# Optimization experiments

Measured on AMD Instinct MI355X. Metric: run time of the kernel, lower is better.

## Reference

```python
import jax, jax.numpy as jnp
import numpy as np

B, N = 1, 320  # embed_dim == seq_len == N is forced by the module's bmm shapes


def setup_inputs() -> dict:
    key = jax.random.key(0)
    k1, k2, k3, k4 = jax.random.split(key, 4)
    s = jax.random.normal(k1, (B, N, N), dtype=jnp.float32)
    futrue = jax.random.normal(k2, (B, N, N, N), dtype=jnp.float32)
    # nn.Linear(embed_dim, embed_dim) params
    lim = 1.0 / np.sqrt(N)
    W = jax.random.uniform(k3, (N, N), minval=-lim, maxval=lim, dtype=jnp.float32)
    b = jax.random.uniform(k4, (N,), minval=-lim, maxval=lim, dtype=jnp.float32)
    return {"s": s, "futrue": futrue, "W": W, "b": b}


def reference(s, futrue, W, b):
    # futrue = self.fc(futrue): Linear on last dim  [B,T,T,E]
    futP = jnp.einsum('bitj,ej->bite', futrue, W) + b
    # fc = s.transpose(1,2) @ futrue : [B,1,E,T] @ [B,T,T,E] -> [B,T,E,E]
    scores = jnp.einsum('bte,bitj->biej', s, futP)
    fc = jax.nn.softmax(scores, axis=-1)          # softmax over last dim
    # vectorized loop: t_i = fc[:, i].sum(1).unsqueeze(-2).bmm(s)
    w = fc.sum(axis=2)                            # [B, T, T] (sum over e)
    out = jnp.einsum('bij,bjk->bik', w, s)        # concat of all t_i -> [B, T, E]
    return out
```

## Files before the change

### kernel.cpp

```cpp
#include <hip/hip_runtime.h>
#include <hip/hip_bf16.h>
#include <math.h>

#define N 320
#define NN (N * N)
#define SST 324

typedef float f32x16 __attribute__((ext_vector_type(16)));
typedef short s16x8  __attribute__((ext_vector_type(8)));

#define MFMA32(a, b, c) __builtin_amdgcn_mfma_f32_32x32x16_bf16((a), (b), (c), 0, 0, 0)

union U4V { uint4 q; s16x8 v; };
union UAV { unsigned u[4]; s16x8 v; };

__device__ inline void split2(float x0, float x1, unsigned& hi, unsigned& lo) {
    unsigned u0 = __float_as_uint(x0), u1 = __float_as_uint(x1);
    hi = (u0 >> 16) | (u1 & 0xFFFF0000u);
    float d0 = x0 - __uint_as_float(u0 & 0xFFFF0000u);
    float d1 = x1 - __uint_as_float(u1 & 0xFFFF0000u);
    lo = (__float_as_uint(d0) >> 16) | (__float_as_uint(d1) & 0xFFFF0000u);
}

__global__ __launch_bounds__(256) void prep_kernel(
    const float* __restrict__ s, const float* __restrict__ W,
    float* __restrict__ wbuf, float* __restrict__ out, float* __restrict__ colsum,
    uint4* __restrict__ spH, uint4* __restrict__ spL,
    uint4* __restrict__ wpH, uint4* __restrict__ wpL)
{
    const int bid = blockIdx.x;
    const int tid = threadIdx.x;
    if (bid < 100) {
        ((float4*)wbuf)[bid * 256 + tid] = make_float4(0.f, 0.f, 0.f, 0.f);
    } else if (bid < 200) {
        ((float4*)out)[(bid - 100) * 256 + tid] = make_float4(0.f, 0.f, 0.f, 0.f);
    } else if (bid < 202) {
        int e = (bid - 200) * 256 + tid;
        if (e < N) {
            const float* sp = s + e;
            float a[8];
#pragma unroll
            for (int u = 0; u < 8; ++u) a[u] = 0.f;
            for (int t = 0; t < N; t += 8) {
#pragma unroll
                for (int u = 0; u < 8; ++u) a[u] += sp[(size_t)(t + u) * N];
            }
            colsum[e] = ((a[0] + a[1]) + (a[2] + a[3])) + ((a[4] + a[5]) + (a[6] + a[7]));
        }
    } else if (bid < 252) {
        int sub = (bid - 202) * 4 + (tid >> 6);
        int l = tid & 63;
        int et = sub / 20, ts = sub % 20;
        int e = et * 32 + (l & 31);
        int t0 = ts * 16 + (l >> 5) * 8;
        unsigned hi[4], lo[4];
#pragma unroll
        for (int d = 0; d < 4; ++d)
            split2(s[(size_t)(t0 + 2 * d) * N + e], s[(size_t)(t0 + 2 * d + 1) * N + e],
                   hi[d], lo[d]);
        spH[sub * 64 + l] = make_uint4(hi[0], hi[1], hi[2], hi[3]);
        spL[sub * 64 + l] = make_uint4(lo[0], lo[1], lo[2], lo[3]);
    } else {
        int sub = (bid - 252) * 4 + (tid >> 6);
        int l = tid & 63;
        int jt = sub / 20, ks = sub % 20;
        int j = jt * 32 + (l & 31);
        int k0 = ks * 16 + (l >> 5) * 8;
        const float* wr = W + (size_t)j * N + k0;
        unsigned hi[4], lo[4];
#pragma unroll
        for (int d = 0; d < 4; ++d) split2(wr[2 * d], wr[2 * d + 1], hi[d], lo[d]);
        wpH[sub * 64 + l] = make_uint4(hi[0], hi[1], hi[2], hi[3]);
        wpL[sub * 64 + l] = make_uint4(lo[0], lo[1], lo[2], lo[3]);
    }
}

__global__ __launch_bounds__(640, 5) void fused5_kernel(
    const float* __restrict__ fut,
    const uint4* __restrict__ spH, const uint4* __restrict__ spL,
    const uint4* __restrict__ wpH, const uint4* __restrict__ wpL,
    const float* __restrict__ bvec, const float* __restrict__ colsum,
    float* __restrict__ w)
{
    const int bid = blockIdx.x;
    const int x  = bid & 7;
    const int g  = bid >> 3;
    const int iw = g / 5, eq = g % 5;
    const int i  = iw * 8 + x;
    const int tid = threadIdx.x;
    const int wid = tid >> 6;
    const int lane = tid & 63;
    const int l31 = lane & 31;
    const int hf  = lane >> 5;

    __shared__ union {
        unsigned short G[2][40 * 32 * 8];
        float S[32 * SST];
    } sm;
    __shared__ float csh[64];
    __shared__ float Mfin[32];
    __shared__ float Ifin[32];

    if (tid < 64) csh[tid] = colsum[eq * 64 + tid];

    f32x16 acc0, acc1;
#pragma unroll
    for (int r = 0; r < 16; ++r) { acc0[r] = 0.f; acc1[r] = 0.f; }

    const float* fbase = fut + (size_t)i * NN + (size_t)(hf * 8) * N + wid * 32 + l31;
    const uint4* aH0 = spH + (size_t)((eq * 2 + 0) * 20) * 64 + lane;
    const uint4* aL0 = spL + (size_t)((eq * 2 + 0) * 20) * 64 + lane;
    const uint4* aH1 = spH + (size_t)((eq * 2 + 1) * 20) * 64 + lane;
    const uint4* aL1 = spL + (size_t)((eq * 2 + 1) * 20) * 64 + lane;

#pragma unroll 2
    for (int ts = 0; ts < 20; ++ts) {
        const float* fp = fbase + (size_t)(ts * 16) * N;
        float f[8];
#pragma unroll
        for (int m = 0; m < 8; ++m) f[m] = fp[(size_t)m * N];
        UAV bh, bl;
#pragma unroll
        for (int d = 0; d < 4; ++d) split2(f[2 * d], f[2 * d + 1], bh.u[d], bl.u[d]);
        U4V a0h, a0l, a1h, a1l;
        a0h.q = aH0[ts * 64]; a0l.q = aL0[ts * 64];
        a1h.q = aH1[ts * 64]; a1l.q = aL1[ts * 64];
        acc0 = MFMA32(a0h.v, bh.v, acc0);
        acc1 = MFMA32(a1h.v, bh.v, acc1);
        acc0 = MFMA32(a0l.v, bh.v, acc0);
        acc1 = MFMA32(a1l.v, bh.v, acc1);
        acc0 = MFMA32(a0h.v, bl.v, acc0);
        acc1 = MFMA32(a1h.v, bl.v, acc1);
    }

    const uint4* bHp = wpH + (size_t)(wid * 20) * 64 + lane;
    const uint4* bLp = wpL + (size_t)(wid * 20) * 64 + lane;
    const int jcol = wid * 32 + l31;
    const float bj = bvec[jcol];
    const int hw = tid >> 5;
    const int li = tid & 31;
    float wcol = 0.f;

    auto doSlab = [&](const f32x16& acc, const int slab) {
        {
            const int c  = wid * 4 + (l31 >> 3);
            const int jj = l31 & 7;
            const int sw = c & 7;
            unsigned short* GH = sm.G[0];
            unsigned short* GL = sm.G[1];
#pragma unroll
            for (int r = 0; r < 16; ++r) {
                int e = (r & 3) + ((r >> 2) << 3) + (hf << 2);
                float xv = acc[r];
                unsigned u = __float_as_uint(xv);
                float d = xv - __uint_as_float(u & 0xFFFF0000u);
                int off = (c * 32 + (e ^ sw)) * 8 + jj;
                GH[off] = (unsigned short)(u >> 16);
                GL[off] = (unsigned short)(__float_as_uint(d) >> 16);
            }
        }
        __syncthreads();

        f32x16 p;
#pragma unroll
        for (int r = 0; r < 16; ++r) p[r] = 0.f;
        const unsigned short* GH = sm.G[0];
        const unsigned short* GL = sm.G[1];
#pragma unroll 4
        for (int ks = 0; ks < 20; ++ks) {
            int c = ks * 2 + hf;
            int off = (c * 32 + (l31 ^ (c & 7))) * 8;
            s16x8 gh = *(const s16x8*)&GH[off];
            s16x8 gl = *(const s16x8*)&GL[off];
            U4V wh, wl;
            wh.q = bHp[ks * 64];
            wl.q = bLp[ks * 64];
            p = MFMA32(gh, wh.v, p);
            p = MFMA32(gl, wh.v, p);
            p = MFMA32(gh, wl.v, p);
        }

        float v[16];
#pragma unroll
        for (int r = 0; r < 16; ++r) {
            int e = (r & 3) + ((r >> 2) << 3) + (hf << 2);
            v[r] = p[r] + csh[slab * 32 + e] * bj;
        }
        __syncthreads();

#pragma unroll
        for (int r = 0; r < 16; ++r) {
            int e = (r & 3) + ((r >> 2) << 3) + (hf << 2);
            sm.S[e * SST + jcol] = v[r];
        }
        __syncthreads();

        if (hw < 16) {
#pragma unroll
            for (int rr = 0; rr < 2; ++rr) {
                int row = 2 * hw + rr;
                float xr[10];
                float m = -3.4e38f;
#pragma unroll
                for (int q = 0; q < 10; ++q) {
                    xr[q] = sm.S[row * SST + li + 32 * q];
                    m = fmaxf(m, xr[q]);
                }
#pragma unroll
                for (int off = 16; off; off >>= 1) m = fmaxf(m, __shfl_xor(m, off, 64));
                float ssum = 0.f;
#pragma unroll
                for (int q = 0; q < 10; ++q) ssum += __expf(xr[q] - m);
#pragma unroll
                for (int off = 16; off; off >>= 1) ssum += __shfl_xor(ssum, off, 64);
                if (li == 0) { Mfin[row] = m; Ifin[row] = 1.0f / ssum; }
            }
        }
        __syncthreads();

#pragma unroll
        for (int r = 0; r < 16; ++r) {
            int e = (r & 3) + ((r >> 2) << 3) + (hf << 2);
            wcol += __expf(v[r] - Mfin[e]) * Ifin[e];
        }
    };

    doSlab(acc0, 0);
    doSlab(acc1, 1);

    wcol += __shfl_xor(wcol, 32, 64);
    if (hf == 0) atomicAdd(&w[(size_t)i * N + jcol], wcol);
}

__global__ __launch_bounds__(320) void out_gemm_kernel(
    const float* __restrict__ w, const float* __restrict__ s,
    float* __restrict__ out)
{
    const int i = blockIdx.x;
    const int jc = blockIdx.y;
    const int k = threadIdx.x;
    const float* wr = w + (size_t)i * N + jc * 80;
    const float* sp = s + (size_t)(jc * 80) * N + k;
    float a0 = 0.f, a1 = 0.f, a2 = 0.f, a3 = 0.f;
    for (int j = 0; j < 80; j += 4) {
        a0 += wr[j + 0] * sp[(size_t)(j + 0) * N];
        a1 += wr[j + 1] * sp[(size_t)(j + 1) * N];
        a2 += wr[j + 2] * sp[(size_t)(j + 2) * N];
        a3 += wr[j + 3] * sp[(size_t)(j + 3) * N];
    }
    atomicAdd(&out[(size_t)i * N + k], (a0 + a1) + (a2 + a3));
}

extern "C" void kernel_launch(void* const* d_in, const int* in_sizes, int n_in,
                              void* d_out, int out_size, void* d_ws, size_t ws_size,
                              hipStream_t stream)
{
    const float* s    = (const float*)d_in[0];
    const float* fut  = (const float*)d_in[1];
    const float* W    = (const float*)d_in[2];
    const float* bvec = (const float*)d_in[3];
    float* out = (float*)d_out;

    char* base = (char*)d_ws;
    float* wbuf   = (float*)base;
    float* colsum = (float*)(base + 409600);
    uint4* spH = (uint4*)(base + 410880);
    uint4* spL = (uint4*)(base + 615680);
    uint4* wpH = (uint4*)(base + 820480);
    uint4* wpL = (uint4*)(base + 1025280);

    prep_kernel<<<dim3(302), dim3(256), 0, stream>>>(
        s, W, wbuf, out, colsum, spH, spL, wpH, wpL);

    fused5_kernel<<<dim3(1600), dim3(640), 0, stream>>>(
        fut, spH, spL, wpH, wpL, bvec, colsum, wbuf);

    out_gemm_kernel<<<dim3(N, 4), dim3(320), 0, stream>>>(wbuf, s, out);
}
```

Baseline: 414.7 us.

## Pre-pack futrue into bf16 hi/lo MFMA fragments in a separate kernel

Adds a packf kernel that reads futrue through shared memory and writes it once as bf16 hi/lo split fragments already in MFMA operand layout. The fused kernel then loads packed fragments instead of doing strided fp32 loads and splitting per block. Each block now handles one 32-row e-tile instead of two, so twice as many blocks run, and the split-precision products use separate accumulators. The cost is an extra 131 MB round-trip (packed hi+lo written then re-read), and each packed fragment is re-read by 10 blocks.

```diff
diff --git a/kernel.cpp b/kernel.cpp
--- a/kernel.cpp
+++ b/kernel.cpp
@@ -12,7 +12,6 @@
 #define MFMA32(a, b, c) __builtin_amdgcn_mfma_f32_32x32x16_bf16((a), (b), (c), 0, 0, 0)
 
 union U4V { uint4 q; s16x8 v; };
-union UAV { unsigned u[4]; s16x8 v; };
 
 __device__ inline void split2(float x0, float x1, unsigned& hi, unsigned& lo) {
     unsigned u0 = __float_as_uint(x0), u1 = __float_as_uint(x1);
@@ -75,18 +74,54 @@
     }
 }
 
-__global__ __launch_bounds__(640, 5) void fused5_kernel(
+__global__ __launch_bounds__(320) void packf_kernel(
     const float* __restrict__ fut,
+    uint4* __restrict__ fpH, uint4* __restrict__ fpL)
+{
+    const int bid = blockIdx.x;
+    const int i = bid / 5, tq = bid % 5;
+    const int t = threadIdx.x;
+    const int l = t & 63, l31 = l & 31, hf = l >> 5;
+    const int jt0 = t >> 6;
+
+    __shared__ float ld[16 * 320];
+
+    for (int tt = 0; tt < 4; ++tt) {
+        const int ts = tq * 4 + tt;
+        const float4* src = (const float4*)(fut + (size_t)i * NN + (size_t)ts * 16 * N);
+        if (tt) __syncthreads();
+#pragma unroll
+        for (int rep = 0; rep < 4; ++rep)
+            ((float4*)ld)[rep * 320 + t] = src[rep * 320 + t];
+        __syncthreads();
+#pragma unroll
+        for (int rr = 0; rr < 2; ++rr) {
+            const int jt = jt0 + rr * 5;
+            const int j = jt * 32 + l31;
+            unsigned hi[4], lo[4];
+#pragma unroll
+            for (int d = 0; d < 4; ++d) {
+                float x0 = ld[(hf * 8 + 2 * d) * 320 + j];
+                float x1 = ld[(hf * 8 + 2 * d + 1) * 320 + j];
+                split2(x0, x1, hi[d], lo[d]);
+            }
+            size_t sub = (size_t)(i * 10 + jt) * 20 + ts;
+            fpH[sub * 64 + l] = make_uint4(hi[0], hi[1], hi[2], hi[3]);
+            fpL[sub * 64 + l] = make_uint4(lo[0], lo[1], lo[2], lo[3]);
+        }
+    }
+}
+
+__global__ __launch_bounds__(640, 5) void fused_kernel(
+    const uint4* __restrict__ fpH, const uint4* __restrict__ fpL,
     const uint4* __restrict__ spH, const uint4* __restrict__ spL,
     const uint4* __restrict__ wpH, const uint4* __restrict__ wpL,
     const float* __restrict__ bvec, const float* __restrict__ colsum,
     float* __restrict__ w)
 {
     const int bid = blockIdx.x;
-    const int x  = bid & 7;
-    const int g  = bid >> 3;
-    const int iw = g / 5, eq = g % 5;
-    const int i  = iw * 8 + x;
+    const int i   = (bid / 80) * 8 + (bid & 7);
+    const int et  = (bid >> 3) % 10;
     const int tid = threadIdx.x;
     const int wid = tid >> 6;
     const int lane = tid & 63;
@@ -97,137 +132,124 @@
         unsigned short G[2][40 * 32 * 8];
         float S[32 * SST];
     } sm;
-    __shared__ float csh[64];
+    __shared__ float csh[32];
     __shared__ float Mfin[32];
     __shared__ float Ifin[32];
 
-    if (tid < 64) csh[tid] = colsum[eq * 64 + tid];
-
-    f32x16 acc0, acc1;
-#pragma unroll
-    for (int r = 0; r < 16; ++r) { acc0[r] = 0.f; acc1[r] = 0.f; }
-
-    const float* fbase = fut + (size_t)i * NN + (size_t)(hf * 8) * N + wid * 32 + l31;
-    const uint4* aH0 = spH + (size_t)((eq * 2 + 0) * 20) * 64 + lane;
-    const uint4* aL0 = spL + (size_t)((eq * 2 + 0) * 20) * 64 + lane;
-    const uint4* aH1 = spH + (size_t)((eq * 2 + 1) * 20) * 64 + lane;
-    const uint4* aL1 = spL + (size_t)((eq * 2 + 1) * 20) * 64 + lane;
+    if (tid < 32) csh[tid] = colsum[et * 32 + tid];
+
+    f32x16 acc1, acc2;
+#pragma unroll
+    for (int r = 0; r < 16; ++r) { acc1[r] = 0.f; acc2[r] = 0.f; }
+
+    const uint4* fH  = fpH + (size_t)((i * 10 + wid) * 20) * 64 + lane;
+    const uint4* fL  = fpL + (size_t)((i * 10 + wid) * 20) * 64 + lane;
+    const uint4* aHp = spH + (size_t)(et * 20) * 64 + lane;
+    const uint4* aLp = spL + (size_t)(et * 20) * 64 + lane;
 
 #pragma unroll 2
     for (int ts = 0; ts < 20; ++ts) {
-        const float* fp = fbase + (size_t)(ts * 16) * N;
-        float f[8];
-#pragma unroll
-        for (int m = 0; m < 8; ++m) f[m] = fp[(size_t)m * N];
-        UAV bh, bl;
-#pragma unroll
-        for (int d = 0; d < 4; ++d) split2(f[2 * d], f[2 * d + 1], bh.u[d], bl.u[d]);
-        U4V a0h, a0l, a1h, a1l;
-        a0h.q = aH0[ts * 64]; a0l.q = aL0[ts * 64];
-        a1h.q = aH1[ts * 64]; a1l.q = aL1[ts * 64];
-        acc0 = MFMA32(a0h.v, bh.v, acc0);
-        acc1 = MFMA32(a1h.v, bh.v, acc1);
-        acc0 = MFMA32(a0l.v, bh.v, acc0);
-        acc1 = MFMA32(a1l.v, bh.v, acc1);
-        acc0 = MFMA32(a0h.v, bl.v, acc0);
-        acc1 = MFMA32(a1h.v, bl.v, acc1);
-    }
+        U4V ah, al, bh, bl;
+        ah.q = aHp[ts * 64];
+        al.q = aLp[ts * 64];
+        bh.q = fH[ts * 64];
+        bl.q = fL[ts * 64];
+        acc1 = MFMA32(ah.v, bh.v, acc1);
+        acc2 = MFMA32(al.v, bh.v, acc2);
+        acc2 = MFMA32(ah.v, bl.v, acc2);
+    }
+
+    {
+        const int c  = wid * 4 + (l31 >> 3);
+        const int jj = l31 & 7;
+        const int sw = c & 7;
+        unsigned short* GH = sm.G[0];
+        unsigned short* GL = sm.G[1];
+#pragma unroll
+        for (int r = 0; r < 16; ++r) {
+            int e = (r & 3) + ((r >> 2) << 3) + (hf << 2);
+            float x = acc1[r] + acc2[r];
+            unsigned u = __float_as_uint(x);
+            float d = x - __uint_as_float(u & 0xFFFF0000u);
+            int off = (c * 32 + (e ^ sw)) * 8 + jj;
+            GH[off] = (unsigned short)(u >> 16);
+            GL[off] = (unsigned short)(__float_as_uint(d) >> 16);
+        }
+    }
+    __syncthreads();
+
+    f32x16 p1, p2;
+#pragma unroll
+    for (int r = 0; r < 16; ++r) { p1[r] = 0.f; p2[r] = 0.f; }
 
     const uint4* bHp = wpH + (size_t)(wid * 20) * 64 + lane;
     const uint4* bLp = wpL + (size_t)(wid * 20) * 64 + lane;
+    const unsigned short* GH = sm.G[0];
+    const unsigned short* GL = sm.G[1];
+
+#pragma unroll 4
+    for (int ks = 0; ks < 20; ++ks) {
+        int c = ks * 2 + hf;
+        int off = (c * 32 + (l31 ^ (c & 7))) * 8;
+        s16x8 gh = *(const s16x8*)&GH[off];
+        s16x8 gl = *(const s16x8*)&GL[off];
+        U4V wh, wl;
+        wh.q = bHp[ks * 64];
+        wl.q = bLp[ks * 64];
+        p1 = MFMA32(gh, wh.v, p1);
+        p2 = MFMA32(gl, wh.v, p2);
+        p2 = MFMA32(gh, wl.v, p2);
+    }
+
     const int jcol = wid * 32 + l31;
-    const float bj = bvec[jcol];
+    float bj = bvec[jcol];
+    float v[16];
+#pragma unroll
+    for (int r = 0; r < 16; ++r) {
+        int e = (r & 3) + ((r >> 2) << 3) + (hf << 2);
+        v[r] = (p1[r] + p2[r]) + csh[e] * bj;
+    }
+
+    __syncthreads();
+
+#pragma unroll
+    for (int r = 0; r < 16; ++r) {
+        int e = (r & 3) + ((r >> 2) << 3) + (hf << 2);
+        sm.S[e * SST + jcol] = v[r];
+    }
+    __syncthreads();
+
     const int hw = tid >> 5;
     const int li = tid & 31;
+    if (hw < 16) {
+#pragma unroll
+        for (int rr = 0; rr < 2; ++rr) {
+            int row = 2 * hw + rr;
+            float x[10];
+            float m = -3.4e38f;
+#pragma unroll
+            for (int q = 0; q < 10; ++q) {
+                x[q] = sm.S[row * SST + li + 32 * q];
+                m = fmaxf(m, x[q]);
+            }
+#pragma unroll
+            for (int off = 16; off; off >>= 1) m = fmaxf(m, __shfl_xor(m, off, 64));
+            float ssum = 0.f;
+#pragma unroll
+            for (int q = 0; q < 10; ++q) ssum += __expf(x[q] - m);
+#pragma unroll
+            for (int off = 16; off; off >>= 1) ssum += __shfl_xor(ssum, off, 64);
+            if (li == 0) { Mfin[row] = m; Ifin[row] = 1.0f / ssum; }
+        }
+    }
+    __syncthreads();
+
     float wcol = 0.f;
-
-    auto doSlab = [&](const f32x16& acc, const int slab) {
-        {
-            const int c  = wid * 4 + (l31 >> 3);
-            const int jj = l31 & 7;
-            const int sw = c & 7;
-            unsigned short* GH = sm.G[0];
-            unsigned short* GL = sm.G[1];
-#pragma unroll
-            for (int r = 0; r < 16; ++r) {
-                int e = (r & 3) + ((r >> 2) << 3) + (hf << 2);
-                float xv = acc[r];
-                unsigned u = __float_as_uint(xv);
-                float d = xv - __uint_as_float(u & 0xFFFF0000u);
-                int off = (c * 32 + (e ^ sw)) * 8 + jj;
-                GH[off] = (unsigned short)(u >> 16);
-                GL[off] = (unsigned short)(__float_as_uint(d) >> 16);
-            }
-        }
-        __syncthreads();
-
-        f32x16 p;
-#pragma unroll
-        for (int r = 0; r < 16; ++r) p[r] = 0.f;
-        const unsigned short* GH = sm.G[0];
-        const unsigned short* GL = sm.G[1];
-#pragma unroll 4
-        for (int ks = 0; ks < 20; ++ks) {
-            int c = ks * 2 + hf;
-            int off = (c * 32 + (l31 ^ (c & 7))) * 8;
-            s16x8 gh = *(const s16x8*)&GH[off];
-            s16x8 gl = *(const s16x8*)&GL[off];
-            U4V wh, wl;
-            wh.q = bHp[ks * 64];
-            wl.q = bLp[ks * 64];
-            p = MFMA32(gh, wh.v, p);
-            p = MFMA32(gl, wh.v, p);
-            p = MFMA32(gh, wl.v, p);
-        }
-
-        float v[16];
-#pragma unroll
-        for (int r = 0; r < 16; ++r) {
-            int e = (r & 3) + ((r >> 2) << 3) + (hf << 2);
-            v[r] = p[r] + csh[slab * 32 + e] * bj;
-        }
-        __syncthreads();
-
-#pragma unroll
-        for (int r = 0; r < 16; ++r) {
-            int e = (r & 3) + ((r >> 2) << 3) + (hf << 2);
-            sm.S[e * SST + jcol] = v[r];
-        }
-        __syncthreads();
-
-        if (hw < 16) {
-#pragma unroll
-            for (int rr = 0; rr < 2; ++rr) {
-                int row = 2 * hw + rr;
-                float xr[10];
-                float m = -3.4e38f;
-#pragma unroll
-                for (int q = 0; q < 10; ++q) {
-                    xr[q] = sm.S[row * SST + li + 32 * q];
-                    m = fmaxf(m, xr[q]);
-                }
-#pragma unroll
-                for (int off = 16; off; off >>= 1) m = fmaxf(m, __shfl_xor(m, off, 64));
-                float ssum = 0.f;
-#pragma unroll
-                for (int q = 0; q < 10; ++q) ssum += __expf(xr[q] - m);
-#pragma unroll
-                for (int off = 16; off; off >>= 1) ssum += __shfl_xor(ssum, off, 64);
-                if (li == 0) { Mfin[row] = m; Ifin[row] = 1.0f / ssum; }
-            }
-        }
-        __syncthreads();
-
-#pragma unroll
-        for (int r = 0; r < 16; ++r) {
-            int e = (r & 3) + ((r >> 2) << 3) + (hf << 2);
-            wcol += __expf(v[r] - Mfin[e]) * Ifin[e];
-        }
-    };
-
-    doSlab(acc0, 0);
-    doSlab(acc1, 1);
-
+#pragma unroll
+    for (int r = 0; r < 16; ++r) {
+        int e = (r & 3) + ((r >> 2) << 3) + (hf << 2);
+        wcol += __expf(v[r] - Mfin[e]) * Ifin[e];
+    }
     wcol += __shfl_xor(wcol, 32, 64);
     if (hf == 0) atomicAdd(&w[(size_t)i * N + jcol], wcol);
 }
@@ -268,12 +290,16 @@
     uint4* spL = (uint4*)(base + 615680);
     uint4* wpH = (uint4*)(base + 820480);
     uint4* wpL = (uint4*)(base + 1025280);
+    uint4* fpH = (uint4*)(base + 1230080);
+    uint4* fpL = (uint4*)(base + 1230080 + 65536000);
 
     prep_kernel<<<dim3(302), dim3(256), 0, stream>>>(
         s, W, wbuf, out, colsum, spH, spL, wpH, wpL);
 
-    fused5_kernel<<<dim3(1600), dim3(640), 0, stream>>>(
-        fut, spH, spL, wpH, wpL, bvec, colsum, wbuf);
+    packf_kernel<<<dim3(1600), dim3(320), 0, stream>>>(fut, fpH, fpL);
+
+    fused_kernel<<<dim3(3200), dim3(640), 0, stream>>>(
+        fpH, fpL, spH, spL, wpH, wpL, bvec, colsum, wbuf);
 
     out_gemm_kernel<<<dim3(N, 4), dim3(320), 0, stream>>>(wbuf, s, out);
 }
```

Result: slower. 429.2 us (+3.5%).

## Process both 32-row slabs together to halve barriers and softmax passes

Applied to the files above, without the earlier changes.

Merges the two sequential per-slab passes (split to bf16, projection GEMM, softmax stats) into one pass over all 64 rows, using 80KB of dynamic shared memory that holds both slabs' hi/lo planes and then a 64x320 score tile. This cuts the number of __syncthreads and lets the projection MFMAs of both slabs interleave with separate accumulators for more ILP. In exchange, shared memory per block roughly doubles and launch bounds drop from 5 to 4 blocks per CU, which lowers occupancy. The padded row stride is also removed, which may add LDS bank conflicts.

```diff
diff --git a/kernel.cpp b/kernel.cpp
--- a/kernel.cpp
+++ b/kernel.cpp
@@ -4,7 +4,6 @@
 
 #define N 320
 #define NN (N * N)
-#define SST 324
 
 typedef float f32x16 __attribute__((ext_vector_type(16)));
 typedef short s16x8  __attribute__((ext_vector_type(8)));
@@ -75,13 +74,17 @@
     }
 }
 
-__global__ __launch_bounds__(640, 5) void fused5_kernel(
+__global__ __launch_bounds__(640, 4) void fused64_kernel(
     const float* __restrict__ fut,
     const uint4* __restrict__ spH, const uint4* __restrict__ spL,
     const uint4* __restrict__ wpH, const uint4* __restrict__ wpL,
     const float* __restrict__ bvec, const float* __restrict__ colsum,
     float* __restrict__ w)
 {
+    extern __shared__ char smraw[];
+    unsigned short* Gsh = (unsigned short*)smraw;
+    float* Ssh = (float*)smraw;
+
     const int bid = blockIdx.x;
     const int x  = bid & 7;
     const int g  = bid >> 3;
@@ -93,16 +96,6 @@
     const int l31 = lane & 31;
     const int hf  = lane >> 5;
 
-    __shared__ union {
-        unsigned short G[2][40 * 32 * 8];
-        float S[32 * SST];
-    } sm;
-    __shared__ float csh[64];
-    __shared__ float Mfin[32];
-    __shared__ float Ifin[32];
-
-    if (tid < 64) csh[tid] = colsum[eq * 64 + tid];
-
     f32x16 acc0, acc1;
 #pragma unroll
     for (int r = 0; r < 16; ++r) { acc0[r] = 0.f; acc1[r] = 0.f; }
@@ -133,101 +126,117 @@
         acc1 = MFMA32(a1h.v, bl.v, acc1);
     }
 
+    {
+        unsigned short* GH0 = Gsh;
+        unsigned short* GL0 = Gsh + 10240;
+        unsigned short* GH1 = Gsh + 20480;
+        unsigned short* GL1 = Gsh + 30720;
+        const int c  = wid * 4 + (l31 >> 3);
+        const int jj = l31 & 7;
+        const int sw = c & 7;
+#pragma unroll
+        for (int r = 0; r < 16; ++r) {
+            int e = (r & 3) + ((r >> 2) << 3) + (hf << 2);
+            int off = (c * 32 + (e ^ sw)) * 8 + jj;
+            {
+                float xv = acc0[r];
+                unsigned u = __float_as_uint(xv);
+                float d = xv - __uint_as_float(u & 0xFFFF0000u);
+                GH0[off] = (unsigned short)(u >> 16);
+                GL0[off] = (unsigned short)(__float_as_uint(d) >> 16);
+            }
+            {
+                float xv = acc1[r];
+                unsigned u = __float_as_uint(xv);
+                float d = xv - __uint_as_float(u & 0xFFFF0000u);
+                GH1[off] = (unsigned short)(u >> 16);
+                GL1[off] = (unsigned short)(__float_as_uint(d) >> 16);
+            }
+        }
+    }
+    __syncthreads();
+
+    f32x16 p0a, p0b, p1a, p1b;
+#pragma unroll
+    for (int r = 0; r < 16; ++r) { p0a[r] = 0.f; p0b[r] = 0.f; p1a[r] = 0.f; p1b[r] = 0.f; }
+
     const uint4* bHp = wpH + (size_t)(wid * 20) * 64 + lane;
     const uint4* bLp = wpL + (size_t)(wid * 20) * 64 + lane;
+    const unsigned short* GH0 = Gsh;
+    const unsigned short* GL0 = Gsh + 10240;
+    const unsigned short* GH1 = Gsh + 20480;
+    const unsigned short* GL1 = Gsh + 30720;
+
+#pragma unroll 2
+    for (int ks = 0; ks < 20; ++ks) {
+        int c = ks * 2 + hf;
+        int off = (c * 32 + (l31 ^ (c & 7))) * 8;
+        s16x8 gh0 = *(const s16x8*)&GH0[off];
+        s16x8 gl0 = *(const s16x8*)&GL0[off];
+        s16x8 gh1 = *(const s16x8*)&GH1[off];
+        s16x8 gl1 = *(const s16x8*)&GL1[off];
+        U4V wh, wl;
+        wh.q = bHp[ks * 64];
+        wl.q = bLp[ks * 64];
+        p0a = MFMA32(gh0, wh.v, p0a);
+        p1a = MFMA32(gh1, wh.v, p1a);
+        p0b = MFMA32(gl0, wh.v, p0b);
+        p1b = MFMA32(gl1, wh.v, p1b);
+        p0b = MFMA32(gh0, wl.v, p0b);
+        p1b = MFMA32(gh1, wl.v, p1b);
+    }
+
     const int jcol = wid * 32 + l31;
     const float bj = bvec[jcol];
+    float v0[16], v1[16];
+#pragma unroll
+    for (int r = 0; r < 16; ++r) {
+        int e = (r & 3) + ((r >> 2) << 3) + (hf << 2);
+        v0[r] = (p0a[r] + p0b[r]) + colsum[eq * 64 + e] * bj;
+        v1[r] = (p1a[r] + p1b[r]) + colsum[eq * 64 + 32 + e] * bj;
+    }
+    __syncthreads();
+
+#pragma unroll
+    for (int r = 0; r < 16; ++r) {
+        int e = (r & 3) + ((r >> 2) << 3) + (hf << 2);
+        Ssh[e * 320 + jcol] = v0[r];
+        Ssh[(32 + e) * 320 + jcol] = v1[r];
+    }
+    __syncthreads();
+
     const int hw = tid >> 5;
     const int li = tid & 31;
+#pragma unroll
+    for (int q = 0; q < 4; ++q) {
+        int row = q * 20 + hw;
+        if (row < 64) {
+            float xr[10];
+            float m = -3.4e38f;
+#pragma unroll
+            for (int k = 0; k < 10; ++k) {
+                xr[k] = Ssh[row * 320 + li + 32 * k];
+                m = fmaxf(m, xr[k]);
+            }
+#pragma unroll
+            for (int off = 16; off; off >>= 1) m = fmaxf(m, __shfl_xor(m, off, 64));
+            float ss = 0.f;
+#pragma unroll
+            for (int k = 0; k < 10; ++k) ss += __expf(xr[k] - m);
+#pragma unroll
+            for (int off = 16; off; off >>= 1) ss += __shfl_xor(ss, off, 64);
+            if (li == 0) { Ssh[row * 320 + 0] = m; Ssh[row * 320 + 1] = 1.0f / ss; }
+        }
+    }
+    __syncthreads();
+
     float wcol = 0.f;
-
-    auto doSlab = [&](const f32x16& acc, const int slab) {
-        {
-            const int c  = wid * 4 + (l31 >> 3);
-            const int jj = l31 & 7;
-            const int sw = c & 7;
-            unsigned short* GH = sm.G[0];
-            unsigned short* GL = sm.G[1];
-#pragma unroll
-            for (int r = 0; r < 16; ++r) {
-                int e = (r & 3) + ((r >> 2) << 3) + (hf << 2);
-                float xv = acc[r];
-                unsigned u = __float_as_uint(xv);
-                float d = xv - __uint_as_float(u & 0xFFFF0000u);
-                int off = (c * 32 + (e ^ sw)) * 8 + jj;
-                GH[off] = (unsigned short)(u >> 16);
-                GL[off] = (unsigned short)(__float_as_uint(d) >> 16);
-            }
-        }
-        __syncthreads();
-
-        f32x16 p;
-#pragma unroll
-        for (int r = 0; r < 16; ++r) p[r] = 0.f;
-        const unsigned short* GH = sm.G[0];
-        const unsigned short* GL = sm.G[1];
-#pragma unroll 4
-        for (int ks = 0; ks < 20; ++ks) {
-            int c = ks * 2 + hf;
-            int off = (c * 32 + (l31 ^ (c & 7))) * 8;
-            s16x8 gh = *(const s16x8*)&GH[off];
-            s16x8 gl = *(const s16x8*)&GL[off];
-            U4V wh, wl;
-            wh.q = bHp[ks * 64];
-            wl.q = bLp[ks * 64];
-            p = MFMA32(gh, wh.v, p);
-            p = MFMA32(gl, wh.v, p);
-            p = MFMA32(gh, wl.v, p);
-        }
-
-        float v[16];
-#pragma unroll
-        for (int r = 0; r < 16; ++r) {
-            int e = (r & 3) + ((r >> 2) << 3) + (hf << 2);
-            v[r] = p[r] + csh[slab * 32 + e] * bj;
-        }
-        __syncthreads();
-
-#pragma unroll
-        for (int r = 0; r < 16; ++r) {
-            int e = (r & 3) + ((r >> 2) << 3) + (hf << 2);
-            sm.S[e * SST + jcol] = v[r];
-        }
-        __syncthreads();
-
-        if (hw < 16) {
-#pragma unroll
-            for (int rr = 0; rr < 2; ++rr) {
-                int row = 2 * hw + rr;
-                float xr[10];
-                float m = -3.4e38f;
-#pragma unroll
-                for (int q = 0; q < 10; ++q) {
-                    xr[q] = sm.S[row * SST + li + 32 * q];
-                    m = fmaxf(m, xr[q]);
-                }
-#pragma unroll
-                for (int off = 16; off; off >>= 1) m = fmaxf(m, __shfl_xor(m, off, 64));
-                float ssum = 0.f;
-#pragma unroll
-                for (int q = 0; q < 10; ++q) ssum += __expf(xr[q] - m);
-#pragma unroll
-                for (int off = 16; off; off >>= 1) ssum += __shfl_xor(ssum, off, 64);
-                if (li == 0) { Mfin[row] = m; Ifin[row] = 1.0f / ssum; }
-            }
-        }
-        __syncthreads();
-
-#pragma unroll
-        for (int r = 0; r < 16; ++r) {
-            int e = (r & 3) + ((r >> 2) << 3) + (hf << 2);
-            wcol += __expf(v[r] - Mfin[e]) * Ifin[e];
-        }
-    };
-
-    doSlab(acc0, 0);
-    doSlab(acc1, 1);
-
+#pragma unroll
+    for (int r = 0; r < 16; ++r) {
+        int e = (r & 3) + ((r >> 2) << 3) + (hf << 2);
+        wcol += __expf(v0[r] - Ssh[e * 320]) * Ssh[e * 320 + 1];
+        wcol += __expf(v1[r] - Ssh[(32 + e) * 320]) * Ssh[(32 + e) * 320 + 1];
+    }
     wcol += __shfl_xor(wcol, 32, 64);
     if (hf == 0) atomicAdd(&w[(size_t)i * N + jcol], wcol);
 }
@@ -269,10 +278,17 @@
     uint4* wpH = (uint4*)(base + 820480);
     uint4* wpL = (uint4*)(base + 1025280);
 
+    static bool attr_done = false;
+    if (!attr_done) {
+        (void)hipFuncSetAttribute((const void*)fused64_kernel,
+                                  hipFuncAttributeMaxDynamicSharedMemorySize, 81920);
+        attr_done = true;
+    }
+
     prep_kernel<<<dim3(302), dim3(256), 0, stream>>>(
         s, W, wbuf, out, colsum, spH, spL, wpH, wpL);
 
-    fused5_kernel<<<dim3(1600), dim3(640), 0, stream>>>(
+    fused64_kernel<<<dim3(1600), dim3(640), 81920, stream>>>(
         fut, spH, spL, wpH, wpL, bvec, colsum, wbuf);
 
     out_gemm_kernel<<<dim3(N, 4), dim3(320), 0, stream>>>(wbuf, s, out);
```

Result: faster. 369.3 us (-11.0%).
